# Optimization experiments

Hardware: AMD Instinct MI355X
Metric: run time of the kernel (lower is better)

Reference implementation:

```python
import jax, jax.numpy as jnp
import numpy as np

N = 100000   # nodes
E = 640000   # directed edges
D = 128      # feature dim
C = 2        # classes


def setup_inputs() -> dict:
    key = jax.random.key(0)
    ks = jax.random.split(key, 7)
    s = 1.0 / np.sqrt(D)
    return {
        "x": jax.random.normal(ks[0], (N, D), jnp.float32),
        "edge_index": jax.random.randint(ks[1], (2, E), 0, N, jnp.int32),
        "W1": jax.random.normal(ks[2], (D, D), jnp.float32) * s,
        "b1": jnp.zeros((D,), jnp.float32),
        "W2": jax.random.normal(ks[3], (D, D), jnp.float32) * s,
        "b2": jnp.zeros((D,), jnp.float32),
        "Wfc": jax.random.normal(ks[4], (D, C), jnp.float32) * s,
        "bfc": jnp.zeros((C,), jnp.float32),
    }


def _gcn_conv(h, src, dst, W, b, n):
    """PyG GCNConv: y = D^{-1/2}(A+I)D^{-1/2} (h @ W) + b."""
    h = h @ W  # [N, D_out]
    loop = jnp.arange(n, dtype=src.dtype)
    s = jnp.concatenate([src, loop])
    d = jnp.concatenate([dst, loop])
    # degree of (A + I) counted at destination
    deg = jax.ops.segment_sum(jnp.ones_like(d, jnp.float32), d, num_segments=n)
    dinv = jax.lax.rsqrt(jnp.maximum(deg, 1.0))  # deg >= 1 via self loops
    norm = dinv[s] * dinv[d]                      # [E+N]
    msg = h[s] * norm[:, None]                    # gather + scale
    out = jax.ops.segment_sum(msg, d, num_segments=n)  # scatter-add
    return out + b


def reference(x, edge_index, W1, b1, W2, b2, Wfc, bfc):
    src, dst = edge_index[0], edge_index[1]
    n = x.shape[0]
    h = jax.nn.relu(_gcn_conv(x, src, dst, W1, b1, n))  # dropout = identity (eval)
    h = jax.nn.relu(_gcn_conv(h, src, dst, W2, b2, n))
    return h @ Wfc + bfc  # [N, 2] logits
```

## Files before the change

### kernel.cpp

```cpp
#include <hip/hip_runtime.h>
#include <hip/hip_bf16.h>

#define D 128
#define NBUCKET 64
#define BCAP 16384

typedef __bf16 bf16x8 __attribute__((ext_vector_type(8)));
typedef float f32x4 __attribute__((ext_vector_type(4)));



__global__ void prep_kernel(const float* __restrict__ W1, const float* __restrict__ W2,
                            __bf16* __restrict__ pw, int* __restrict__ bucket_cursor) {
    int b = blockIdx.x;
    if (b < 128) {
        int t = b * 256 + threadIdx.x;
        int which = t >> 14, idx = t & 16383;
        const float* W = which ? W2 : W1;
        float w = W[idx];
        int k = idx >> 7, nn = idx & 127;
        int ks = which ? (((k & 15) << 3) | (k >> 4)) : k;
        int ntile = nn >> 4, nl = nn & 15;
        int kchunk = ks >> 5, quad = (ks >> 3) & 3, j = ks & 7;
        int o = (((ntile * 4 + kchunk) * 64 + quad * 16 + nl) << 3) + j;
        pw[(size_t)which * 16384 + o] = (__bf16)w;
    } else {
        if (threadIdx.x < NBUCKET) bucket_cursor[threadIdx.x] = 0;
    }
}


__global__ void mega1_kernel(const float* __restrict__ X, const __bf16* __restrict__ PW,
                             __bf16* __restrict__ Zs, int nrows, int gb,
                             const int* __restrict__ src, const int* __restrict__ dst,
                             int* __restrict__ bucket_cursor, int2* __restrict__ bucket_edges,
                             int e, int bucketW) {
    __shared__ __align__(16) char smem[32768];
    int t = threadIdx.x;
    int b = blockIdx.x;
    if (b >= gb) {
        int* hist = (int*)smem;
        int* gbase = hist + 64;
        if (t < NBUCKET) hist[t] = 0;
        __syncthreads();
        int i0 = ((b - gb) * 256 + t) * 4;
        int sv[4], dv[4], bk[4], ls[4];
        int nv = 0;
        if (i0 + 4 <= e) {
            int4 s4 = *(const int4*)(src + i0);
            int4 d4 = *(const int4*)(dst + i0);
            sv[0] = s4.x; sv[1] = s4.y; sv[2] = s4.z; sv[3] = s4.w;
            dv[0] = d4.x; dv[1] = d4.y; dv[2] = d4.z; dv[3] = d4.w;
            nv = 4;
        } else {
            for (int i = i0; i < e; i++) { sv[nv] = src[i]; dv[nv] = dst[i]; nv++; }
        }
        for (int u = 0; u < nv; u++) {
            bk[u] = dv[u] / bucketW;
            ls[u] = atomicAdd(&hist[bk[u]], 1);
        }
        __syncthreads();
        if (t < NBUCKET) gbase[t] = atomicAdd(&bucket_cursor[t], hist[t]);
        __syncthreads();
        for (int u = 0; u < nv; u++) {
            int pos = bk[u] * BCAP + gbase[bk[u]] + ls[u];
            bucket_edges[pos] = make_int2(sv[u], dv[u]);
        }
        return;
    }
    bf16x8* sB = (bf16x8*)smem;
    const bf16x8* PW8 = (const bf16x8*)PW;
#pragma unroll
    for (int i = 0; i < 8; i++) sB[t + 256 * i] = PW8[t + 256 * i];

    int wave = t >> 6, lane = t & 63;
    int qm = lane & 15, quad = lane >> 4;
    int r0 = b * 64 + wave * 16;
    int row = r0 + qm;
    bool valid = row < nrows;
    const float* xr = X + (size_t)row * D + quad * 8;

    bf16x8 ahi[4], alo[4];
#pragma unroll
    for (int c = 0; c < 4; c++) {
        float4 zf = {0.f, 0.f, 0.f, 0.f};
        float4 xa = valid ? ((const float4*)(xr + c * 32))[0] : zf;
        float4 xb = valid ? ((const float4*)(xr + c * 32))[1] : zf;
        float xs[8] = {xa.x, xa.y, xa.z, xa.w, xb.x, xb.y, xb.z, xb.w};
        bf16x8 h, l;
#pragma unroll
        for (int j = 0; j < 8; j++) {
            float v = xs[j];
            __bf16 hh = (__bf16)v;
            h[j] = hh;
            l[j] = (__bf16)(v - (float)hh);
        }
        ahi[c] = h; alo[c] = l;
    }

    f32x4 acc[8];
#pragma unroll
    for (int nt = 0; nt < 8; nt++) acc[nt] = (f32x4){0.f, 0.f, 0.f, 0.f};

    __syncthreads();

#pragma unroll
    for (int c = 0; c < 4; c++) {
#pragma unroll
        for (int nt = 0; nt < 8; nt++) {
            bf16x8 bb = sB[(nt * 4 + c) * 64 + lane];
            acc[nt] = __builtin_amdgcn_mfma_f32_16x16x32_bf16(ahi[c], bb, acc[nt], 0, 0, 0);
            acc[nt] = __builtin_amdgcn_mfma_f32_16x16x32_bf16(alo[c], bb, acc[nt], 0, 0, 0);
        }
    }

#pragma unroll
    for (int reg = 0; reg < 4; reg++) {
        int orow = r0 + quad * 4 + reg;
        if (orow < nrows) {
            bf16x8 o;
#pragma unroll
            for (int nt = 0; nt < 8; nt++) o[nt] = (__bf16)acc[nt][reg];
            *(bf16x8*)(Zs + (size_t)orow * D + qm * 8) = o;
        }
    }
}


__global__ void count_kernel(const int2* __restrict__ bucket_edges,
                             const int* __restrict__ bucket_cursor,
                             int* __restrict__ counts, int n, int bucketW, int subW) {
    __shared__ int bins[400];
    int b = blockIdx.x, t = threadIdx.x;
    int bk = b >> 2, j = b & 3;
    int ns = bk * bucketW + j * subW;
    int be = min((bk + 1) * bucketW, n);
    int ne = min(ns + subW, be);
    if (ns >= ne) return;
    int w = ne - ns;
    for (int i = t; i < w; i += 256) bins[i] = 0;
    __syncthreads();
    int m = bucket_cursor[bk];
    const int2* eb = bucket_edges + (size_t)bk * BCAP;
    for (int i = t; i < m; i += 256) {
        int d = eb[i].y;
        if (d >= ns && d < ne) atomicAdd(&bins[d - ns], 1);
    }
    __syncthreads();
    for (int i = t; i < w; i += 256) counts[ns + i] = bins[i];
}


__global__ void scan_part(const int* __restrict__ counts, int* __restrict__ partial, int n) {
    __shared__ int sm[256];
    int b = blockIdx.x, t = threadIdx.x;
    int base = b * 2048 + t * 8;
    int s = 0;
#pragma unroll
    for (int j = 0; j < 8; j++) { int idx = base + j; if (idx < n) s += counts[idx]; }
    sm[t] = s; __syncthreads();
    for (int off = 128; off > 0; off >>= 1) { if (t < off) sm[t] += sm[t + off]; __syncthreads(); }
    if (t == 0) partial[b] = sm[0];
}

__global__ void scan_top(int* partial, int nb) {
    __shared__ int sm[256];
    int t = threadIdx.x;
    int v = (t < nb) ? partial[t] : 0;
    sm[t] = v; __syncthreads();
    for (int off = 1; off < 256; off <<= 1) {
        int u = (t >= off) ? sm[t - off] : 0;
        __syncthreads();
        sm[t] += u;
        __syncthreads();
    }
    if (t < nb) partial[t] = sm[t] - v;
}

__global__ void scan_down(const int* __restrict__ counts, const int* __restrict__ blockoff,
                          int* __restrict__ row_ptr, float* __restrict__ dinv, int n) {
    __shared__ int sm[256];
    int b = blockIdx.x, t = threadIdx.x;
    int base = b * 2048 + t * 8;
    int c[8], local[8];
    int s = 0;
#pragma unroll
    for (int j = 0; j < 8; j++) {
        int idx = base + j;
        c[j] = (idx < n) ? counts[idx] : 0;
        local[j] = s; s += c[j];
        if (idx < n) dinv[idx] = rsqrtf((float)(c[j] + 1));
    }
    sm[t] = s; __syncthreads();
    int own = s;
    for (int off = 1; off < 256; off <<= 1) {
        int u = (t >= off) ? sm[t - off] : 0;
        __syncthreads();
        sm[t] += u;
        __syncthreads();
    }
    int basev = blockoff[b] + sm[t] - own;
#pragma unroll
    for (int j = 0; j < 8; j++) { int idx = base + j; if (idx < n) row_ptr[idx] = basev + local[j]; }
}


__global__ void fill_kernel(const int2* __restrict__ bucket_edges,
                            const int* __restrict__ bucket_cursor,
                            const int* __restrict__ row_ptr, int* __restrict__ csr,
                            int n, int bucketW, int subW) {
    __shared__ int cur[400];
    int b = blockIdx.x, t = threadIdx.x;
    int bk = b >> 2, j = b & 3;
    int ns = bk * bucketW + j * subW;
    int be = min((bk + 1) * bucketW, n);
    int ne = min(ns + subW, be);
    if (ns >= ne) return;
    int w = ne - ns;
    for (int i = t; i < w; i += 256) cur[i] = row_ptr[ns + i];
    __syncthreads();
    int m = bucket_cursor[bk];
    const int2* eb = bucket_edges + (size_t)bk * BCAP;
    for (int i = t; i < m; i += 256) {
        int2 ed = eb[i];
        if (ed.y >= ns && ed.y < ne) {
            int pos = atomicAdd(&cur[ed.y - ns], 1);
            csr[pos] = ed.x;
        }
    }
}


__global__ void gemm2_mfma(const __bf16* __restrict__ Hs, const __bf16* __restrict__ PW,
                           __bf16* __restrict__ Zs, int nrows) {
    __shared__ bf16x8 sB[2048];
    int t = threadIdx.x;
    const bf16x8* PW8 = (const bf16x8*)PW;
#pragma unroll
    for (int i = 0; i < 8; i++) sB[t + 256 * i] = PW8[t + 256 * i];

    int wave = t >> 6, lane = t & 63;
    int qm = lane & 15, quad = lane >> 4;
    int r0 = blockIdx.x * 64 + wave * 16;
    int row = r0 + qm;
    bool valid = row < nrows;
    const __bf16* hr = Hs + (size_t)row * D + quad * 8;

    bf16x8 a[4];
#pragma unroll
    for (int c = 0; c < 4; c++) {
        bf16x8 z8 = {};
        a[c] = valid ? *(const bf16x8*)(hr + c * 32) : z8;
    }

    f32x4 acc[8];
#pragma unroll
    for (int nt = 0; nt < 8; nt++) acc[nt] = (f32x4){0.f, 0.f, 0.f, 0.f};

    __syncthreads();

#pragma unroll
    for (int c = 0; c < 4; c++) {
#pragma unroll
        for (int nt = 0; nt < 8; nt++) {
            bf16x8 b = sB[(nt * 4 + c) * 64 + lane];
            acc[nt] = __builtin_amdgcn_mfma_f32_16x16x32_bf16(a[c], b, acc[nt], 0, 0, 0);
        }
    }

#pragma unroll
    for (int reg = 0; reg < 4; reg++) {
        int orow = r0 + quad * 4 + reg;
        if (orow < nrows) {
            bf16x8 o;
#pragma unroll
            for (int nt = 0; nt < 8; nt++) o[nt] = (__bf16)acc[nt][reg];
            *(bf16x8*)(Zs + (size_t)orow * D + qm * 8) = o;
        }
    }
}


__global__ void agg1_kernel(const __bf16* __restrict__ Zs, const int* __restrict__ row_ptr,
                            const int* __restrict__ counts, const int* __restrict__ csr,
                            const float* __restrict__ dinv, const float* __restrict__ bias,
                            __bf16* __restrict__ Hs, int n) {
    int t = blockIdx.x * 256 + threadIdx.x;
    int v = t >> 4, c = t & 15;
    if (v >= n) return;
    float dv = dinv[v];
    const bf16x8* Z8 = (const bf16x8*)Zs;
    bf16x8 zc = Z8[(size_t)v * 16 + c];
    float sw = dv * dv;
    float acc[8];
#pragma unroll
    for (int j = 0; j < 8; j++) acc[j] = (float)zc[j] * sw;
    int start = row_ptr[v], cnt = counts[v];
    int i = 0;
    for (; i + 4 <= cnt; i += 4) {
        int s0 = csr[start + i], s1 = csr[start + i + 1];
        int s2 = csr[start + i + 2], s3 = csr[start + i + 3];
        bf16x8 m0 = Z8[(size_t)s0 * 16 + c];
        bf16x8 m1 = Z8[(size_t)s1 * 16 + c];
        bf16x8 m2 = Z8[(size_t)s2 * 16 + c];
        bf16x8 m3 = Z8[(size_t)s3 * 16 + c];
        float w0 = dinv[s0] * dv, w1 = dinv[s1] * dv;
        float w2 = dinv[s2] * dv, w3 = dinv[s3] * dv;
#pragma unroll
        for (int j = 0; j < 8; j++) acc[j] = fmaf(w0, (float)m0[j], acc[j]);
#pragma unroll
        for (int j = 0; j < 8; j++) acc[j] = fmaf(w1, (float)m1[j], acc[j]);
#pragma unroll
        for (int j = 0; j < 8; j++) acc[j] = fmaf(w2, (float)m2[j], acc[j]);
#pragma unroll
        for (int j = 0; j < 8; j++) acc[j] = fmaf(w3, (float)m3[j], acc[j]);
    }
    for (; i < cnt; i++) {
        int s0 = csr[start + i];
        float w0 = dinv[s0] * dv;
        bf16x8 m0 = Z8[(size_t)s0 * 16 + c];
#pragma unroll
        for (int j = 0; j < 8; j++) acc[j] = fmaf(w0, (float)m0[j], acc[j]);
    }
    bf16x8 o;
#pragma unroll
    for (int j = 0; j < 8; j++) o[j] = (__bf16)fmaxf(acc[j] + bias[j * 16 + c], 0.f);
    ((bf16x8*)Hs)[(size_t)v * 16 + c] = o;
}


__global__ void agg2_fc_kernel(const __bf16* __restrict__ Zs, const int* __restrict__ row_ptr,
                               const int* __restrict__ counts, const int* __restrict__ csr,
                               const float* __restrict__ dinv, const float* __restrict__ bias,
                               const float* __restrict__ Wfc, const float* __restrict__ bfc,
                               float* __restrict__ out, int n) {
    int t = blockIdx.x * 256 + threadIdx.x;
    int v = t >> 4, c = t & 15;
    if (v >= n) return;
    float dv = dinv[v];
    const bf16x8* Z8 = (const bf16x8*)Zs;
    bf16x8 zc = Z8[(size_t)v * 16 + c];
    float sw = dv * dv;
    float acc[8];
#pragma unroll
    for (int j = 0; j < 8; j++) acc[j] = (float)zc[j] * sw;
    int start = row_ptr[v], cnt = counts[v];
    int i = 0;
    for (; i + 4 <= cnt; i += 4) {
        int s0 = csr[start + i], s1 = csr[start + i + 1];
        int s2 = csr[start + i + 2], s3 = csr[start + i + 3];
        bf16x8 m0 = Z8[(size_t)s0 * 16 + c];
        bf16x8 m1 = Z8[(size_t)s1 * 16 + c];
        bf16x8 m2 = Z8[(size_t)s2 * 16 + c];
        bf16x8 m3 = Z8[(size_t)s3 * 16 + c];
        float w0 = dinv[s0] * dv, w1 = dinv[s1] * dv;
        float w2 = dinv[s2] * dv, w3 = dinv[s3] * dv;
#pragma unroll
        for (int j = 0; j < 8; j++) acc[j] = fmaf(w0, (float)m0[j], acc[j]);
#pragma unroll
        for (int j = 0; j < 8; j++) acc[j] = fmaf(w1, (float)m1[j], acc[j]);
#pragma unroll
        for (int j = 0; j < 8; j++) acc[j] = fmaf(w2, (float)m2[j], acc[j]);
#pragma unroll
        for (int j = 0; j < 8; j++) acc[j] = fmaf(w3, (float)m3[j], acc[j]);
    }
    for (; i < cnt; i++) {
        int s0 = csr[start + i];
        float w0 = dinv[s0] * dv;
        bf16x8 m0 = Z8[(size_t)s0 * 16 + c];
#pragma unroll
        for (int j = 0; j < 8; j++) acc[j] = fmaf(w0, (float)m0[j], acc[j]);
    }
    float a0 = 0.f, a1 = 0.f;
#pragma unroll
    for (int j = 0; j < 8; j++) {
        int p = j * 16 + c;
        float hj = fmaxf(acc[j] + bias[p], 0.f);
        a0 = fmaf(hj, Wfc[p * 2], a0);
        a1 = fmaf(hj, Wfc[p * 2 + 1], a1);
    }
#pragma unroll
    for (int off = 8; off > 0; off >>= 1) {
        a0 += __shfl_down(a0, off, 16);
        a1 += __shfl_down(a1, off, 16);
    }
    if (c == 0) {
        out[(size_t)v * 2 + 0] = a0 + bfc[0];
        out[(size_t)v * 2 + 1] = a1 + bfc[1];
    }
}


extern "C" void kernel_launch(void* const* d_in, const int* in_sizes, int n_in,
                              void* d_out, int out_size, void* d_ws, size_t ws_size,
                              hipStream_t stream) {
    const float* x   = (const float*)d_in[0];
    const int*   ei  = (const int*)d_in[1];
    const float* W1  = (const float*)d_in[2];
    const float* b1  = (const float*)d_in[3];
    const float* W2  = (const float*)d_in[4];
    const float* b2  = (const float*)d_in[5];
    const float* Wfc = (const float*)d_in[6];
    const float* bfc = (const float*)d_in[7];
    float* out = (float*)d_out;

    int n = in_sizes[0] / D;
    int e = in_sizes[1] / 2;
    const int* src = ei;
    const int* dst = ei + e;

    int bucketW = (n + NBUCKET - 1) / NBUCKET;
    int subW = (bucketW + 3) / 4;

    char* ws = (char*)d_ws;
    size_t nb = (size_t)n * 4;
    int*    counts  = (int*)(ws);
    float*  dinv    = (float*)(ws + nb);
    int*    rowptr  = (int*)(ws + 2 * nb);
    int*    partial = (int*)(ws + 3 * nb);
    int*    bcur    = (int*)(ws + 3 * nb + 1024);
    int2*   bedges  = (int2*)(ws + 3 * nb + 2048);
    size_t  off1    = 3 * nb + 2048 + (size_t)NBUCKET * BCAP * 8;
    int*    csr     = (int*)(ws + off1);
    __bf16* pw      = (__bf16*)(ws + off1 + (size_t)e * 4);
    __bf16* z1      = (__bf16*)(ws + off1 + (size_t)e * 4 + 65536);
    __bf16* h1      = z1 + (size_t)n * D;
    __bf16* z2      = h1 + (size_t)n * D;

    int eab = ((e + 3) / 4 + 255) / 256;
    int sb  = (n + 2047) / 2048;
    int gb  = (n + 63) / 64;
    int ab  = ((n * 16) + 255) / 256;

    prep_kernel<<<129, 256, 0, stream>>>(W1, W2, pw, bcur);
    mega1_kernel<<<gb + eab, 256, 0, stream>>>(x, pw, z1, n, gb, src, dst,
                                               bcur, bedges, e, bucketW);
    count_kernel<<<256, 256, 0, stream>>>(bedges, bcur, counts, n, bucketW, subW);
    scan_part<<<sb, 256, 0, stream>>>(counts, partial, n);
    scan_top<<<1, 256, 0, stream>>>(partial, sb);
    scan_down<<<sb, 256, 0, stream>>>(counts, partial, rowptr, dinv, n);
    fill_kernel<<<256, 256, 0, stream>>>(bedges, bcur, rowptr, csr, n, bucketW, subW);

    agg1_kernel<<<ab, 256, 0, stream>>>(z1, rowptr, counts, csr, dinv, b1, h1, n);
    gemm2_mfma<<<gb, 256, 0, stream>>>(h1, pw + 16384, z2, n);
    agg2_fc_kernel<<<ab, 256, 0, stream>>>(z2, rowptr, counts, csr, dinv, b2, Wfc, bfc, out, n);
}
```

Measured before the change: 241.5 us.

## Fuse CSR build scan into count/fill and layer-1 aggregation into GEMM2

```diff
diff --git a/kernel.cpp b/kernel.cpp
--- a/kernel.cpp
+++ b/kernel.cpp
@@ -7,7 +7,6 @@
 
 typedef __bf16 bf16x8 __attribute__((ext_vector_type(8)));
 typedef float f32x4 __attribute__((ext_vector_type(4)));
-
 
 
 __global__ void prep_kernel(const float* __restrict__ W1, const float* __restrict__ W2,
@@ -29,7 +28,6 @@
     }
 }
 
-
 __global__ void mega1_kernel(const float* __restrict__ X, const __bf16* __restrict__ PW,
                              __bf16* __restrict__ Zs, int nrows, int gb,
                              const int* __restrict__ src, const int* __restrict__ dst,
@@ -126,18 +124,19 @@
     }
 }
 
-
-__global__ void count_kernel(const int2* __restrict__ bucket_edges,
-                             const int* __restrict__ bucket_cursor,
-                             int* __restrict__ counts, int n, int bucketW, int subW) {
+__global__ void count2_kernel(const int2* __restrict__ bucket_edges,
+                              const int* __restrict__ bucket_cursor,
+                              int* __restrict__ counts, float* __restrict__ dinv,
+                              int* __restrict__ partial, int n, int bucketW, int subW) {
     __shared__ int bins[400];
+    __shared__ int sm[256];
     int b = blockIdx.x, t = threadIdx.x;
     int bk = b >> 2, j = b & 3;
     int ns = bk * bucketW + j * subW;
     int be = min((bk + 1) * bucketW, n);
     int ne = min(ns + subW, be);
-    if (ns >= ne) return;
     int w = ne - ns;
+    if (w <= 0) { if (t == 0) partial[b] = 0; return; }
     for (int i = t; i < w; i += 256) bins[i] = 0;
     __syncthreads();
     int m = bucket_cursor[bk];
@@ -147,17 +146,13 @@
         if (d >= ns && d < ne) atomicAdd(&bins[d - ns], 1);
     }
     __syncthreads();
-    for (int i = t; i < w; i += 256) counts[ns + i] = bins[i];
-}
-
-
-__global__ void scan_part(const int* __restrict__ counts, int* __restrict__ partial, int n) {
-    __shared__ int sm[256];
-    int b = blockIdx.x, t = threadIdx.x;
-    int base = b * 2048 + t * 8;
     int s = 0;
-#pragma unroll
-    for (int j = 0; j < 8; j++) { int idx = base + j; if (idx < n) s += counts[idx]; }
+    for (int i = t; i < w; i += 256) {
+        int c = bins[i];
+        counts[ns + i] = c;
+        dinv[ns + i] = rsqrtf((float)(c + 1));
+        s += c;
+    }
     sm[t] = s; __syncthreads();
     for (int off = 128; off > 0; off >>= 1) { if (t < off) sm[t] += sm[t + off]; __syncthreads(); }
     if (t == 0) partial[b] = sm[0];
@@ -177,47 +172,35 @@
     if (t < nb) partial[t] = sm[t] - v;
 }
 
-__global__ void scan_down(const int* __restrict__ counts, const int* __restrict__ blockoff,
-                          int* __restrict__ row_ptr, float* __restrict__ dinv, int n) {
+__global__ void scanfill_kernel(const int2* __restrict__ bucket_edges,
+                                const int* __restrict__ bucket_cursor,
+                                const int* __restrict__ counts,
+                                const int* __restrict__ partial,
+                                int* __restrict__ row_ptr, int* __restrict__ csr,
+                                int n, int bucketW, int subW) {
+    __shared__ int cur[400];
     __shared__ int sm[256];
-    int b = blockIdx.x, t = threadIdx.x;
-    int base = b * 2048 + t * 8;
-    int c[8], local[8];
-    int s = 0;
-#pragma unroll
-    for (int j = 0; j < 8; j++) {
-        int idx = base + j;
-        c[j] = (idx < n) ? counts[idx] : 0;
-        local[j] = s; s += c[j];
-        if (idx < n) dinv[idx] = rsqrtf((float)(c[j] + 1));
-    }
-    sm[t] = s; __syncthreads();
-    int own = s;
-    for (int off = 1; off < 256; off <<= 1) {
-        int u = (t >= off) ? sm[t - off] : 0;
-        __syncthreads();
-        sm[t] += u;
-        __syncthreads();
-    }
-    int basev = blockoff[b] + sm[t] - own;
-#pragma unroll
-    for (int j = 0; j < 8; j++) { int idx = base + j; if (idx < n) row_ptr[idx] = basev + local[j]; }
-}
-
-
-__global__ void fill_kernel(const int2* __restrict__ bucket_edges,
-                            const int* __restrict__ bucket_cursor,
-                            const int* __restrict__ row_ptr, int* __restrict__ csr,
-                            int n, int bucketW, int subW) {
-    __shared__ int cur[400];
     int b = blockIdx.x, t = threadIdx.x;
     int bk = b >> 2, j = b & 3;
     int ns = bk * bucketW + j * subW;
     int be = min((bk + 1) * bucketW, n);
     int ne = min(ns + subW, be);
-    if (ns >= ne) return;
     int w = ne - ns;
-    for (int i = t; i < w; i += 256) cur[i] = row_ptr[ns + i];
+    if (w <= 0) return;
+    int i0 = t * 2;
+    int c0 = (i0 < w) ? counts[ns + i0] : 0;
+    int c1 = (i0 + 1 < w) ? counts[ns + i0 + 1] : 0;
+    sm[t] = c0 + c1; __syncthreads();
+    int own = c0 + c1;
+    for (int off = 1; off < 256; off <<= 1) {
+        int u = (t >= off) ? sm[t - off] : 0;
+        __syncthreads();
+        sm[t] += u;
+        __syncthreads();
+    }
+    int base = partial[b] + sm[t] - own;
+    if (i0 < w)     { row_ptr[ns + i0] = base;          cur[i0] = base; }
+    if (i0 + 1 < w) { row_ptr[ns + i0 + 1] = base + c0; cur[i0 + 1] = base + c0; }
     __syncthreads();
     int m = bucket_cursor[bk];
     const int2* eb = bucket_edges + (size_t)bk * BCAP;
@@ -230,104 +213,93 @@
     }
 }
 
-
-__global__ void gemm2_mfma(const __bf16* __restrict__ Hs, const __bf16* __restrict__ PW,
-                           __bf16* __restrict__ Zs, int nrows) {
-    __shared__ bf16x8 sB[2048];
+__global__ void agg1gemm2_kernel(const __bf16* __restrict__ Zs, const int* __restrict__ row_ptr,
+                                 const int* __restrict__ counts, const int* __restrict__ csr,
+                                 const float* __restrict__ dinv, const float* __restrict__ bias,
+                                 const __bf16* __restrict__ PW2, __bf16* __restrict__ Z2, int n) {
+    __shared__ bf16x8 htile[64][17];
     int t = threadIdx.x;
-    const bf16x8* PW8 = (const bf16x8*)PW;
-#pragma unroll
-    for (int i = 0; i < 8; i++) sB[t + 256 * i] = PW8[t + 256 * i];
+    int r0 = blockIdx.x * 64;
+    const bf16x8* Z8 = (const bf16x8*)Zs;
+    int c = t & 15;
+    int nsub = t >> 4;
+#pragma unroll
+    for (int rd = 0; rd < 4; rd++) {
+        int v = r0 + rd * 16 + nsub;
+        bf16x8 o = {};
+        if (v < n) {
+            float dv = dinv[v];
+            bf16x8 zc = Z8[(size_t)v * 16 + c];
+            float sw = dv * dv;
+            float acc[8];
+#pragma unroll
+            for (int jj = 0; jj < 8; jj++) acc[jj] = (float)zc[jj] * sw;
+            int start = row_ptr[v], cnt = counts[v];
+            int i = 0;
+            for (; i + 4 <= cnt; i += 4) {
+                int s0 = csr[start + i], s1 = csr[start + i + 1];
+                int s2 = csr[start + i + 2], s3 = csr[start + i + 3];
+                bf16x8 m0 = Z8[(size_t)s0 * 16 + c];
+                bf16x8 m1 = Z8[(size_t)s1 * 16 + c];
+                bf16x8 m2 = Z8[(size_t)s2 * 16 + c];
+                bf16x8 m3 = Z8[(size_t)s3 * 16 + c];
+                float w0 = dinv[s0] * dv, w1 = dinv[s1] * dv;
+                float w2 = dinv[s2] * dv, w3 = dinv[s3] * dv;
+#pragma unroll
+                for (int jj = 0; jj < 8; jj++) acc[jj] = fmaf(w0, (float)m0[jj], acc[jj]);
+#pragma unroll
+                for (int jj = 0; jj < 8; jj++) acc[jj] = fmaf(w1, (float)m1[jj], acc[jj]);
+#pragma unroll
+                for (int jj = 0; jj < 8; jj++) acc[jj] = fmaf(w2, (float)m2[jj], acc[jj]);
+#pragma unroll
+                for (int jj = 0; jj < 8; jj++) acc[jj] = fmaf(w3, (float)m3[jj], acc[jj]);
+            }
+            for (; i < cnt; i++) {
+                int s0 = csr[start + i];
+                float w0 = dinv[s0] * dv;
+                bf16x8 m0 = Z8[(size_t)s0 * 16 + c];
+#pragma unroll
+                for (int jj = 0; jj < 8; jj++) acc[jj] = fmaf(w0, (float)m0[jj], acc[jj]);
+            }
+#pragma unroll
+            for (int jj = 0; jj < 8; jj++) o[jj] = (__bf16)fmaxf(acc[jj] + bias[jj * 16 + c], 0.f);
+        }
+        htile[rd * 16 + nsub][c] = o;
+    }
+    __syncthreads();
 
     int wave = t >> 6, lane = t & 63;
     int qm = lane & 15, quad = lane >> 4;
-    int r0 = blockIdx.x * 64 + wave * 16;
-    int row = r0 + qm;
-    bool valid = row < nrows;
-    const __bf16* hr = Hs + (size_t)row * D + quad * 8;
-
+    int rowl = wave * 16 + qm;
     bf16x8 a[4];
 #pragma unroll
-    for (int c = 0; c < 4; c++) {
-        bf16x8 z8 = {};
-        a[c] = valid ? *(const bf16x8*)(hr + c * 32) : z8;
-    }
-
-    f32x4 acc[8];
-#pragma unroll
-    for (int nt = 0; nt < 8; nt++) acc[nt] = (f32x4){0.f, 0.f, 0.f, 0.f};
-
-    __syncthreads();
-
-#pragma unroll
-    for (int c = 0; c < 4; c++) {
+    for (int c4 = 0; c4 < 4; c4++) a[c4] = htile[rowl][c4 * 4 + quad];
+
+    f32x4 acc2[8];
+#pragma unroll
+    for (int nt = 0; nt < 8; nt++) acc2[nt] = (f32x4){0.f, 0.f, 0.f, 0.f};
+
+    const bf16x8* B8 = (const bf16x8*)PW2;
+#pragma unroll
+    for (int c4 = 0; c4 < 4; c4++) {
 #pragma unroll
         for (int nt = 0; nt < 8; nt++) {
-            bf16x8 b = sB[(nt * 4 + c) * 64 + lane];
-            acc[nt] = __builtin_amdgcn_mfma_f32_16x16x32_bf16(a[c], b, acc[nt], 0, 0, 0);
+            bf16x8 bb = B8[(nt * 4 + c4) * 64 + lane];
+            acc2[nt] = __builtin_amdgcn_mfma_f32_16x16x32_bf16(a[c4], bb, acc2[nt], 0, 0, 0);
         }
     }
 
 #pragma unroll
     for (int reg = 0; reg < 4; reg++) {
-        int orow = r0 + quad * 4 + reg;
-        if (orow < nrows) {
+        int orow = r0 + wave * 16 + quad * 4 + reg;
+        if (orow < n) {
             bf16x8 o;
 #pragma unroll
-            for (int nt = 0; nt < 8; nt++) o[nt] = (__bf16)acc[nt][reg];
-            *(bf16x8*)(Zs + (size_t)orow * D + qm * 8) = o;
-        }
-    }
-}
-
-
-__global__ void agg1_kernel(const __bf16* __restrict__ Zs, const int* __restrict__ row_ptr,
-                            const int* __restrict__ counts, const int* __restrict__ csr,
-                            const float* __restrict__ dinv, const float* __restrict__ bias,
-                            __bf16* __restrict__ Hs, int n) {
-    int t = blockIdx.x * 256 + threadIdx.x;
-    int v = t >> 4, c = t & 15;
-    if (v >= n) return;
-    float dv = dinv[v];
-    const bf16x8* Z8 = (const bf16x8*)Zs;
-    bf16x8 zc = Z8[(size_t)v * 16 + c];
-    float sw = dv * dv;
-    float acc[8];
-#pragma unroll
-    for (int j = 0; j < 8; j++) acc[j] = (float)zc[j] * sw;
-    int start = row_ptr[v], cnt = counts[v];
-    int i = 0;
-    for (; i + 4 <= cnt; i += 4) {
-        int s0 = csr[start + i], s1 = csr[start + i + 1];
-        int s2 = csr[start + i + 2], s3 = csr[start + i + 3];
-        bf16x8 m0 = Z8[(size_t)s0 * 16 + c];
-        bf16x8 m1 = Z8[(size_t)s1 * 16 + c];
-        bf16x8 m2 = Z8[(size_t)s2 * 16 + c];
-        bf16x8 m3 = Z8[(size_t)s3 * 16 + c];
-        float w0 = dinv[s0] * dv, w1 = dinv[s1] * dv;
-        float w2 = dinv[s2] * dv, w3 = dinv[s3] * dv;
-#pragma unroll
-        for (int j = 0; j < 8; j++) acc[j] = fmaf(w0, (float)m0[j], acc[j]);
-#pragma unroll
-        for (int j = 0; j < 8; j++) acc[j] = fmaf(w1, (float)m1[j], acc[j]);
-#pragma unroll
-        for (int j = 0; j < 8; j++) acc[j] = fmaf(w2, (float)m2[j], acc[j]);
-#pragma unroll
-        for (int j = 0; j < 8; j++) acc[j] = fmaf(w3, (float)m3[j], acc[j]);
-    }
-    for (; i < cnt; i++) {
-        int s0 = csr[start + i];
-        float w0 = dinv[s0] * dv;
-        bf16x8 m0 = Z8[(size_t)s0 * 16 + c];
-#pragma unroll
-        for (int j = 0; j < 8; j++) acc[j] = fmaf(w0, (float)m0[j], acc[j]);
-    }
-    bf16x8 o;
-#pragma unroll
-    for (int j = 0; j < 8; j++) o[j] = (__bf16)fmaxf(acc[j] + bias[j * 16 + c], 0.f);
-    ((bf16x8*)Hs)[(size_t)v * 16 + c] = o;
-}
-
+            for (int nt = 0; nt < 8; nt++) o[nt] = (__bf16)acc2[nt][reg];
+            *(bf16x8*)(Z2 + (size_t)orow * D + qm * 8) = o;
+        }
+    }
+}
 
 __global__ void agg2_fc_kernel(const __bf16* __restrict__ Zs, const int* __restrict__ row_ptr,
                                const int* __restrict__ counts, const int* __restrict__ csr,
@@ -424,24 +396,20 @@
     int*    csr     = (int*)(ws + off1);
     __bf16* pw      = (__bf16*)(ws + off1 + (size_t)e * 4);
     __bf16* z1      = (__bf16*)(ws + off1 + (size_t)e * 4 + 65536);
-    __bf16* h1      = z1 + (size_t)n * D;
-    __bf16* z2      = h1 + (size_t)n * D;
+    __bf16* z2      = z1 + (size_t)n * D;
 
     int eab = ((e + 3) / 4 + 255) / 256;
-    int sb  = (n + 2047) / 2048;
     int gb  = (n + 63) / 64;
     int ab  = ((n * 16) + 255) / 256;
 
     prep_kernel<<<129, 256, 0, stream>>>(W1, W2, pw, bcur);
     mega1_kernel<<<gb + eab, 256, 0, stream>>>(x, pw, z1, n, gb, src, dst,
                                                bcur, bedges, e, bucketW);
-    count_kernel<<<256, 256, 0, stream>>>(bedges, bcur, counts, n, bucketW, subW);
-    scan_part<<<sb, 256, 0, stream>>>(counts, partial, n);
-    scan_top<<<1, 256, 0, stream>>>(partial, sb);
-    scan_down<<<sb, 256, 0, stream>>>(counts, partial, rowptr, dinv, n);
-    fill_kernel<<<256, 256, 0, stream>>>(bedges, bcur, rowptr, csr, n, bucketW, subW);
-
-    agg1_kernel<<<ab, 256, 0, stream>>>(z1, rowptr, counts, csr, dinv, b1, h1, n);
-    gemm2_mfma<<<gb, 256, 0, stream>>>(h1, pw + 16384, z2, n);
+    count2_kernel<<<256, 256, 0, stream>>>(bedges, bcur, counts, dinv, partial, n, bucketW, subW);
+    scan_top<<<1, 256, 0, stream>>>(partial, 256);
+    scanfill_kernel<<<256, 256, 0, stream>>>(bedges, bcur, counts, partial, rowptr, csr,
+                                             n, bucketW, subW);
+    agg1gemm2_kernel<<<gb, 256, 0, stream>>>(z1, rowptr, counts, csr, dinv, b1,
+                                             pw + 16384, z2, n);
     agg2_fc_kernel<<<ab, 256, 0, stream>>>(z2, rowptr, counts, csr, dinv, b2, Wfc, bfc, out, n);
 }
```

Measured after the change: 240.3 us. About the same (-0.5%).

## Fuse CSR scan into count/fill kernels and degree-sort nodes for aggregation

Applied to the files above, without the earlier changes.

```diff
diff --git a/kernel.cpp b/kernel.cpp
--- a/kernel.cpp
+++ b/kernel.cpp
@@ -9,9 +9,9 @@
 typedef float f32x4 __attribute__((ext_vector_type(4)));
 
 
-
 __global__ void prep_kernel(const float* __restrict__ W1, const float* __restrict__ W2,
-                            __bf16* __restrict__ pw, int* __restrict__ bucket_cursor) {
+                            __bf16* __restrict__ pw, int* __restrict__ bucket_cursor,
+                            int* __restrict__ deghist) {
     int b = blockIdx.x;
     if (b < 128) {
         int t = b * 256 + threadIdx.x;
@@ -25,10 +25,11 @@
         int o = (((ntile * 4 + kchunk) * 64 + quad * 16 + nl) << 3) + j;
         pw[(size_t)which * 16384 + o] = (__bf16)w;
     } else {
-        if (threadIdx.x < NBUCKET) bucket_cursor[threadIdx.x] = 0;
-    }
-}
-
+        int t = threadIdx.x;
+        if (t < NBUCKET) bucket_cursor[t] = 0;
+        else if (t < 128) deghist[t - 64] = 0;
+    }
+}
 
 __global__ void mega1_kernel(const float* __restrict__ X, const __bf16* __restrict__ PW,
                              __bf16* __restrict__ Zs, int nrows, int gb,
@@ -126,19 +127,23 @@
     }
 }
 
-
-__global__ void count_kernel(const int2* __restrict__ bucket_edges,
-                             const int* __restrict__ bucket_cursor,
-                             int* __restrict__ counts, int n, int bucketW, int subW) {
+__global__ void count2_kernel(const int2* __restrict__ bucket_edges,
+                              const int* __restrict__ bucket_cursor,
+                              int* __restrict__ counts, float* __restrict__ dinv,
+                              int* __restrict__ partial, int* __restrict__ deghist,
+                              int n, int bucketW, int subW) {
     __shared__ int bins[400];
+    __shared__ int sm[256];
+    __shared__ int hb[64];
     int b = blockIdx.x, t = threadIdx.x;
     int bk = b >> 2, j = b & 3;
     int ns = bk * bucketW + j * subW;
     int be = min((bk + 1) * bucketW, n);
     int ne = min(ns + subW, be);
-    if (ns >= ne) return;
     int w = ne - ns;
+    if (w <= 0) { if (t == 0) partial[b] = 0; return; }
     for (int i = t; i < w; i += 256) bins[i] = 0;
+    if (t < 64) hb[t] = 0;
     __syncthreads();
     int m = bucket_cursor[bk];
     const int2* eb = bucket_edges + (size_t)bk * BCAP;
@@ -147,23 +152,21 @@
         if (d >= ns && d < ne) atomicAdd(&bins[d - ns], 1);
     }
     __syncthreads();
-    for (int i = t; i < w; i += 256) counts[ns + i] = bins[i];
-}
-
-
-__global__ void scan_part(const int* __restrict__ counts, int* __restrict__ partial, int n) {
-    __shared__ int sm[256];
-    int b = blockIdx.x, t = threadIdx.x;
-    int base = b * 2048 + t * 8;
     int s = 0;
-#pragma unroll
-    for (int j = 0; j < 8; j++) { int idx = base + j; if (idx < n) s += counts[idx]; }
+    for (int i = t; i < w; i += 256) {
+        int c = bins[i];
+        counts[ns + i] = c;
+        dinv[ns + i] = rsqrtf((float)(c + 1));
+        atomicAdd(&hb[min(c, 63)], 1);
+        s += c;
+    }
     sm[t] = s; __syncthreads();
     for (int off = 128; off > 0; off >>= 1) { if (t < off) sm[t] += sm[t + off]; __syncthreads(); }
     if (t == 0) partial[b] = sm[0];
-}
-
-__global__ void scan_top(int* partial, int nb) {
+    if (t < 64 && hb[t]) atomicAdd(&deghist[t], hb[t]);
+}
+
+__global__ void scan_top(int* partial, int* deghist, int* degcur, int nb) {
     __shared__ int sm[256];
     int t = threadIdx.x;
     int v = (t < nb) ? partial[t] : 0;
@@ -175,49 +178,59 @@
         __syncthreads();
     }
     if (t < nb) partial[t] = sm[t] - v;
-}
-
-__global__ void scan_down(const int* __restrict__ counts, const int* __restrict__ blockoff,
-                          int* __restrict__ row_ptr, float* __restrict__ dinv, int n) {
+    __syncthreads();
+    int d = (t < 64) ? deghist[t] : 0;
+    sm[t] = d; __syncthreads();
+    for (int off = 1; off < 64; off <<= 1) {
+        int u = (t >= off && t < 64) ? sm[t - off] : 0;
+        __syncthreads();
+        if (t < 64) sm[t] += u;
+        __syncthreads();
+    }
+    if (t < 64) degcur[t] = sm[t] - d;
+}
+
+__global__ void scanfill_kernel(const int2* __restrict__ bucket_edges,
+                                const int* __restrict__ bucket_cursor,
+                                const int* __restrict__ counts,
+                                const int* __restrict__ partial,
+                                int* __restrict__ row_ptr, int* __restrict__ csr,
+                                int* __restrict__ degcur, int* __restrict__ order,
+                                int n, int bucketW, int subW) {
+    __shared__ int cur[400];
     __shared__ int sm[256];
-    int b = blockIdx.x, t = threadIdx.x;
-    int base = b * 2048 + t * 8;
-    int c[8], local[8];
-    int s = 0;
-#pragma unroll
-    for (int j = 0; j < 8; j++) {
-        int idx = base + j;
-        c[j] = (idx < n) ? counts[idx] : 0;
-        local[j] = s; s += c[j];
-        if (idx < n) dinv[idx] = rsqrtf((float)(c[j] + 1));
-    }
-    sm[t] = s; __syncthreads();
-    int own = s;
-    for (int off = 1; off < 256; off <<= 1) {
-        int u = (t >= off) ? sm[t - off] : 0;
-        __syncthreads();
-        sm[t] += u;
-        __syncthreads();
-    }
-    int basev = blockoff[b] + sm[t] - own;
-#pragma unroll
-    for (int j = 0; j < 8; j++) { int idx = base + j; if (idx < n) row_ptr[idx] = basev + local[j]; }
-}
-
-
-__global__ void fill_kernel(const int2* __restrict__ bucket_edges,
-                            const int* __restrict__ bucket_cursor,
-                            const int* __restrict__ row_ptr, int* __restrict__ csr,
-                            int n, int bucketW, int subW) {
-    __shared__ int cur[400];
+    __shared__ int hb2[64];
+    __shared__ int gb2[64];
     int b = blockIdx.x, t = threadIdx.x;
     int bk = b >> 2, j = b & 3;
     int ns = bk * bucketW + j * subW;
     int be = min((bk + 1) * bucketW, n);
     int ne = min(ns + subW, be);
-    if (ns >= ne) return;
     int w = ne - ns;
-    for (int i = t; i < w; i += 256) cur[i] = row_ptr[ns + i];
+    if (w <= 0) return;
+    if (t < 64) hb2[t] = 0;
+    int i0 = t * 2;
+    int c0 = (i0 < w) ? counts[ns + i0] : 0;
+    int c1 = (i0 + 1 < w) ? counts[ns + i0 + 1] : 0;
+    sm[t] = c0 + c1; __syncthreads();
+    int own = c0 + c1;
+    for (int off = 1; off < 256; off <<= 1) {
+        int u = (t >= off) ? sm[t - off] : 0;
+        __syncthreads();
+        sm[t] += u;
+        __syncthreads();
+    }
+    int base = partial[b] + sm[t] - own;
+    if (i0 < w)     { row_ptr[ns + i0] = base;          cur[i0] = base; }
+    if (i0 + 1 < w) { row_ptr[ns + i0 + 1] = base + c0; cur[i0 + 1] = base + c0; }
+    int bin0 = min(c0, 63), bin1 = min(c1, 63);
+    int r0 = (i0 < w) ? atomicAdd(&hb2[bin0], 1) : 0;
+    int r1 = (i0 + 1 < w) ? atomicAdd(&hb2[bin1], 1) : 0;
+    __syncthreads();
+    if (t < 64 && hb2[t]) gb2[t] = atomicAdd(&degcur[t], hb2[t]);
+    __syncthreads();
+    if (i0 < w)     order[gb2[bin0] + r0] = ns + i0;
+    if (i0 + 1 < w) order[gb2[bin1] + r1] = ns + i0 + 1;
     __syncthreads();
     int m = bucket_cursor[bk];
     const int2* eb = bucket_edges + (size_t)bk * BCAP;
@@ -230,64 +243,14 @@
     }
 }
 
-
-__global__ void gemm2_mfma(const __bf16* __restrict__ Hs, const __bf16* __restrict__ PW,
-                           __bf16* __restrict__ Zs, int nrows) {
-    __shared__ bf16x8 sB[2048];
-    int t = threadIdx.x;
-    const bf16x8* PW8 = (const bf16x8*)PW;
-#pragma unroll
-    for (int i = 0; i < 8; i++) sB[t + 256 * i] = PW8[t + 256 * i];
-
-    int wave = t >> 6, lane = t & 63;
-    int qm = lane & 15, quad = lane >> 4;
-    int r0 = blockIdx.x * 64 + wave * 16;
-    int row = r0 + qm;
-    bool valid = row < nrows;
-    const __bf16* hr = Hs + (size_t)row * D + quad * 8;
-
-    bf16x8 a[4];
-#pragma unroll
-    for (int c = 0; c < 4; c++) {
-        bf16x8 z8 = {};
-        a[c] = valid ? *(const bf16x8*)(hr + c * 32) : z8;
-    }
-
-    f32x4 acc[8];
-#pragma unroll
-    for (int nt = 0; nt < 8; nt++) acc[nt] = (f32x4){0.f, 0.f, 0.f, 0.f};
-
-    __syncthreads();
-
-#pragma unroll
-    for (int c = 0; c < 4; c++) {
-#pragma unroll
-        for (int nt = 0; nt < 8; nt++) {
-            bf16x8 b = sB[(nt * 4 + c) * 64 + lane];
-            acc[nt] = __builtin_amdgcn_mfma_f32_16x16x32_bf16(a[c], b, acc[nt], 0, 0, 0);
-        }
-    }
-
-#pragma unroll
-    for (int reg = 0; reg < 4; reg++) {
-        int orow = r0 + quad * 4 + reg;
-        if (orow < nrows) {
-            bf16x8 o;
-#pragma unroll
-            for (int nt = 0; nt < 8; nt++) o[nt] = (__bf16)acc[nt][reg];
-            *(bf16x8*)(Zs + (size_t)orow * D + qm * 8) = o;
-        }
-    }
-}
-
-
 __global__ void agg1_kernel(const __bf16* __restrict__ Zs, const int* __restrict__ row_ptr,
                             const int* __restrict__ counts, const int* __restrict__ csr,
                             const float* __restrict__ dinv, const float* __restrict__ bias,
-                            __bf16* __restrict__ Hs, int n) {
+                            const int* __restrict__ order, __bf16* __restrict__ Hs, int n) {
     int t = blockIdx.x * 256 + threadIdx.x;
-    int v = t >> 4, c = t & 15;
-    if (v >= n) return;
+    int idx = t >> 4, c = t & 15;
+    if (idx >= n) return;
+    int v = order[idx];
     float dv = dinv[v];
     const bf16x8* Z8 = (const bf16x8*)Zs;
     bf16x8 zc = Z8[(size_t)v * 16 + c];
@@ -328,15 +291,64 @@
     ((bf16x8*)Hs)[(size_t)v * 16 + c] = o;
 }
 
+__global__ void gemm2_mfma(const __bf16* __restrict__ Hs, const __bf16* __restrict__ PW,
+                           __bf16* __restrict__ Zs, int nrows) {
+    __shared__ bf16x8 sB[2048];
+    int t = threadIdx.x;
+    const bf16x8* PW8 = (const bf16x8*)PW;
+#pragma unroll
+    for (int i = 0; i < 8; i++) sB[t + 256 * i] = PW8[t + 256 * i];
+
+    int wave = t >> 6, lane = t & 63;
+    int qm = lane & 15, quad = lane >> 4;
+    int r0 = blockIdx.x * 64 + wave * 16;
+    int row = r0 + qm;
+    bool valid = row < nrows;
+    const __bf16* hr = Hs + (size_t)row * D + quad * 8;
+
+    bf16x8 a[4];
+#pragma unroll
+    for (int c = 0; c < 4; c++) {
+        bf16x8 z8 = {};
+        a[c] = valid ? *(const bf16x8*)(hr + c * 32) : z8;
+    }
+
+    f32x4 acc[8];
+#pragma unroll
+    for (int nt = 0; nt < 8; nt++) acc[nt] = (f32x4){0.f, 0.f, 0.f, 0.f};
+
+    __syncthreads();
+
+#pragma unroll
+    for (int c = 0; c < 4; c++) {
+#pragma unroll
+        for (int nt = 0; nt < 8; nt++) {
+            bf16x8 b = sB[(nt * 4 + c) * 64 + lane];
+            acc[nt] = __builtin_amdgcn_mfma_f32_16x16x32_bf16(a[c], b, acc[nt], 0, 0, 0);
+        }
+    }
+
+#pragma unroll
+    for (int reg = 0; reg < 4; reg++) {
+        int orow = r0 + quad * 4 + reg;
+        if (orow < nrows) {
+            bf16x8 o;
+#pragma unroll
+            for (int nt = 0; nt < 8; nt++) o[nt] = (__bf16)acc[nt][reg];
+            *(bf16x8*)(Zs + (size_t)orow * D + qm * 8) = o;
+        }
+    }
+}
 
 __global__ void agg2_fc_kernel(const __bf16* __restrict__ Zs, const int* __restrict__ row_ptr,
                                const int* __restrict__ counts, const int* __restrict__ csr,
                                const float* __restrict__ dinv, const float* __restrict__ bias,
                                const float* __restrict__ Wfc, const float* __restrict__ bfc,
-                               float* __restrict__ out, int n) {
+                               const int* __restrict__ order, float* __restrict__ out, int n) {
     int t = blockIdx.x * 256 + threadIdx.x;
-    int v = t >> 4, c = t & 15;
-    if (v >= n) return;
+    int idx = t >> 4, c = t & 15;
+    if (idx >= n) return;
+    int v = order[idx];
     float dv = dinv[v];
     const bf16x8* Z8 = (const bf16x8*)Zs;
     bf16x8 zc = Z8[(size_t)v * 16 + c];
@@ -419,8 +431,11 @@
     int*    rowptr  = (int*)(ws + 2 * nb);
     int*    partial = (int*)(ws + 3 * nb);
     int*    bcur    = (int*)(ws + 3 * nb + 1024);
-    int2*   bedges  = (int2*)(ws + 3 * nb + 2048);
-    size_t  off1    = 3 * nb + 2048 + (size_t)NBUCKET * BCAP * 8;
+    int*    deghist = (int*)(ws + 3 * nb + 1280);
+    int*    degcur  = (int*)(ws + 3 * nb + 1536);
+    int*    order   = (int*)(ws + 3 * nb + 2048);
+    int2*   bedges  = (int2*)(ws + 4 * nb + 2048);
+    size_t  off1    = 4 * nb + 2048 + (size_t)NBUCKET * BCAP * 8;
     int*    csr     = (int*)(ws + off1);
     __bf16* pw      = (__bf16*)(ws + off1 + (size_t)e * 4);
     __bf16* z1      = (__bf16*)(ws + off1 + (size_t)e * 4 + 65536);
@@ -428,20 +443,19 @@
     __bf16* z2      = h1 + (size_t)n * D;
 
     int eab = ((e + 3) / 4 + 255) / 256;
-    int sb  = (n + 2047) / 2048;
     int gb  = (n + 63) / 64;
     int ab  = ((n * 16) + 255) / 256;
 
-    prep_kernel<<<129, 256, 0, stream>>>(W1, W2, pw, bcur);
+    prep_kernel<<<129, 256, 0, stream>>>(W1, W2, pw, bcur, deghist);
     mega1_kernel<<<gb + eab, 256, 0, stream>>>(x, pw, z1, n, gb, src, dst,
                                                bcur, bedges, e, bucketW);
-    count_kernel<<<256, 256, 0, stream>>>(bedges, bcur, counts, n, bucketW, subW);
-    scan_part<<<sb, 256, 0, stream>>>(counts, partial, n);
-    scan_top<<<1, 256, 0, stream>>>(partial, sb);
-    scan_down<<<sb, 256, 0, stream>>>(counts, partial, rowptr, dinv, n);
-    fill_kernel<<<256, 256, 0, stream>>>(bedges, bcur, rowptr, csr, n, bucketW, subW);
-
-    agg1_kernel<<<ab, 256, 0, stream>>>(z1, rowptr, counts, csr, dinv, b1, h1, n);
+    count2_kernel<<<256, 256, 0, stream>>>(bedges, bcur, counts, dinv, partial, deghist,
+                                           n, bucketW, subW);
+    scan_top<<<1, 256, 0, stream>>>(partial, deghist, degcur, 256);
+    scanfill_kernel<<<256, 256, 0, stream>>>(bedges, bcur, counts, partial, rowptr, csr,
+                                             degcur, order, n, bucketW, subW);
+    agg1_kernel<<<ab, 256, 0, stream>>>(z1, rowptr, counts, csr, dinv, b1, order, h1, n);
     gemm2_mfma<<<gb, 256, 0, stream>>>(h1, pw + 16384, z2, n);
-    agg2_fc_kernel<<<ab, 256, 0, stream>>>(z2, rowptr, counts, csr, dinv, b2, Wfc, bfc, out, n);
-}
+    agg2_fc_kernel<<<ab, 256, 0, stream>>>(z2, rowptr, counts, csr, dinv, b2, Wfc, bfc,
+                                           order, out, n);
+}
```

After: 237.8 us. About the same (-1.5%).
